# Kernel tuning notes

Hardware: AMD Instinct MI355X
Metric: run time of the kernel (lower is better)

Reference implementation:

```python
import jax, jax.numpy as jnp
import numpy as np

N = 10000      # nodes
E = 320000     # edges (before self loops)
IN = 256
HID = 64
H = 8
OUT = 64
NEG_SLOPE = 0.2


def setup_inputs() -> dict:
    key = jax.random.key(0)
    ks = jax.random.split(key, 12)
    def glorot(k, shape):
        fan = sum(shape) if len(shape) == 2 else int(np.prod(shape))
        return jax.random.normal(k, shape, jnp.float32) * np.sqrt(2.0 / fan)
    x = jax.random.normal(ks[0], (N, IN), jnp.float32)
    edge_index = jax.random.randint(ks[1], (2, E), 0, N, jnp.int32)
    # positive weights so log2 is finite
    edge_weight = jax.random.uniform(ks[2], (E,), jnp.float32, 0.1, 1.0)
    return {
        'x': x, 'edge_index': edge_index, 'edge_weight': edge_weight,
        'W1': glorot(ks[3], (IN, H * HID)),
        'as1': glorot(ks[4], (H, HID)), 'ad1': glorot(ks[5], (H, HID)),
        'b1': jnp.zeros((H * HID,), jnp.float32),
        'W2': glorot(ks[6], (H * HID, H * OUT)),
        'as2': glorot(ks[7], (H, OUT)), 'ad2': glorot(ks[8], (H, OUT)),
        'b2': jnp.zeros((H * OUT,), jnp.float32),
    }


def _gat_conv(x, src, dst, log2_ew, W, att_src, att_dst, bias, heads, ch):
    n = x.shape[0]
    h = (x @ W).reshape(n, heads, ch)                      # [N,H,C]
    al_src = jnp.einsum('nhc,hc->nh', h, att_src)          # [N,H]
    al_dst = jnp.einsum('nhc,hc->nh', h, att_dst)
    alpha = al_src[src] + al_dst[dst]                      # [E,H]
    alpha = jax.nn.leaky_relu(alpha, NEG_SLOPE)
    alpha = alpha + log2_ew[:, None]
    # segment softmax over destination nodes (self loops ensure nonempty segments)
    amax = jax.ops.segment_max(alpha, dst, num_segments=n)
    ex = jnp.exp(alpha - amax[dst])
    denom = jax.ops.segment_sum(ex, dst, num_segments=n)
    alpha = ex / denom[dst]                                # [E,H]
    msg = h[src] * alpha[:, :, None]                       # [E,H,C]
    out = jax.ops.segment_sum(msg, dst, num_segments=n)    # [N,H,C]
    return out.reshape(n, heads * ch) + bias


def reference(x, edge_index, edge_weight, W1, as1, ad1, b1, W2, as2, ad2, b2):
    n = x.shape[0]
    # add self loops with fill_value = 1.0 (log2(1) = 0)
    loops = jnp.arange(n, dtype=edge_index.dtype)
    src = jnp.concatenate([edge_index[0], loops])
    dst = jnp.concatenate([edge_index[1], loops])
    ew = jnp.concatenate([edge_weight, jnp.ones((n,), edge_weight.dtype)])
    log2_ew = jnp.log2(ew)
    h = _gat_conv(x, src, dst, log2_ew, W1, as1, ad1, b1, H, HID)
    h = jax.nn.relu(h)  # dropout skipped (eval mode)
    out = _gat_conv(h, src, dst, log2_ew, W2, as2, ad2, b2, H, OUT)
    return out
```

## Files before the change

### kernel.cpp

```cpp
#include <hip/hip_runtime.h>
#include <hip/hip_bf16.h>

#define NN 10000
#define EE 320000
#define ETOT (EE + NN)
#define CIN 256
#define HC 512
#define NHEAD 8
#define NEG 0.2f

#define SX (NN * CIN)
#define SATT (6 * 512)

using bf16x8 = __attribute__((ext_vector_type(8))) short;
using f32x4 = __attribute__((ext_vector_type(4))) float;
typedef unsigned short u16;
typedef unsigned int u32;

__device__ __forceinline__ u16 f2bf(float f) {
  __hip_bfloat16 b = __float2bfloat16(f);
  return *(u16*)&b;
}
__device__ __forceinline__ float bflo(u32 p) { return __uint_as_float(p << 16); }
__device__ __forceinline__ float bfhi(u32 p) { return __uint_as_float(p & 0xFFFF0000u); }

#define PB_X ((SX + 255) / 256)
#define PB_ATT ((SATT + 255) / 256)
#define PB_CNT ((ETOT + 255) / 256)
#define PB_WT 96
#define PB_TOT (PB_X + PB_ATT + PB_CNT + PB_WT)

__global__ __launch_bounds__(256) void prep_k(
    const void* __restrict__ x, const void* __restrict__ w1,
    const void* __restrict__ w2,
    const void* a0, const void* a1, const void* a2,
    const void* a3, const void* a4, const void* a5,
    const int* __restrict__ ei,
    u16* __restrict__ xb, u16* __restrict__ w1t, u16* __restrict__ w2t,
    float* __restrict__ attf, int* __restrict__ counts, int* __restrict__ flag) {
  const int b = blockIdx.x, t = threadIdx.x;
  __shared__ int sbad;
  if (t == 0) sbad = 0;
  __syncthreads();
  {
    const u16* xu = (const u16*)x;
    unsigned e0 = (xu[2 * t] >> 7) & 0xFFu;
    unsigned e1 = (xu[2 * t + 1] >> 7) & 0xFFu;
    if (e0 >= 0xC8u || e1 >= 0xC8u) sbad = 1;
  }
  __syncthreads();
  const bool bf = (sbad == 0);
  if (b == 0 && t == 0) *flag = bf ? 1 : 0;

  if (b < PB_X) {
    if (!bf) {
      int i = b * 256 + t;
      if (i < SX) xb[i] = f2bf(((const float*)x)[i]);
    }
  } else if (b < PB_X + PB_ATT) {
    int j = (b - PB_X) * 256 + t;
    if (j < SATT) {
      const void* ps[6] = {a0, a1, a2, a3, a4, a5};
      const void* p = ps[j >> 9];
      int k = j & 511;
      attf[j] = bf ? __bfloat162float(((const __hip_bfloat16*)p)[k])
                   : ((const float*)p)[k];
    }
  } else if (b < PB_X + PB_ATT + PB_CNT) {
    int e = (b - PB_X - PB_ATT) * 256 + t;
    if (e < ETOT) {
      int d = (e < EE) ? ei[EE + e] : (e - EE);
      atomicAdd(&counts[d], 1);
    }
  } else {
    __shared__ u16 tile[64][72];
    int wb = b - (PB_X + PB_ATT + PB_CNT);
    const void* src;
    u16* dst;
    int K, tk, tn;
    if (wb < 32) { src = w1; dst = w1t; K = CIN; tk = (wb >> 3) * 64; tn = (wb & 7) * 64; }
    else { wb -= 32; src = w2; dst = w2t; K = HC; tk = (wb >> 3) * 64; tn = (wb & 7) * 64; }
    const int r = t >> 2, cb = (t & 3) * 16;
    if (bf) {
      const u16* s = (const u16*)src + (size_t)(tk + r) * HC + tn + cb;
      *(int4*)&tile[r][cb] = ((const int4*)s)[0];
      *(int4*)&tile[r][cb + 8] = ((const int4*)s)[1];
    } else {
      const float* s = (const float*)src + (size_t)(tk + r) * HC + tn + cb;
#pragma unroll
      for (int j = 0; j < 16; j++) tile[r][cb + j] = f2bf(s[j]);
    }
    __syncthreads();
    union { u16 o[16]; int4 v[2]; } u;
#pragma unroll
    for (int j = 0; j < 16; j++) u.o[j] = tile[cb + j][r];
    int4* dp = (int4*)(dst + (size_t)(tn + r) * K + tk + cb);
    dp[0] = u.v[0];
    dp[1] = u.v[1];
  }
}

__global__ __launch_bounds__(1024) void scan_k(const int* __restrict__ counts,
                                               int* __restrict__ rowptr,
                                               int* __restrict__ wcur) {
  __shared__ int buf[1024];
  const int t = threadIdx.x;
  int loc[10];
  int s = 0;
#pragma unroll
  for (int j = 0; j < 10; j++) {
    int i = t * 10 + j;
    s += (i < NN) ? counts[i] : 0;
    loc[j] = s;
  }
  buf[t] = s;
  __syncthreads();
  for (int off = 1; off < 1024; off <<= 1) {
    int v = (t >= off) ? buf[t - off] : 0;
    __syncthreads();
    buf[t] += v;
    __syncthreads();
  }
  int base = (t > 0) ? buf[t - 1] : 0;
  int prev = 0;
#pragma unroll
  for (int j = 0; j < 10; j++) {
    int i = t * 10 + j;
    if (i < NN) {
      rowptr[i + 1] = base + loc[j];
      wcur[i] = base + prev;
    }
    prev = loc[j];
  }
  if (t == 0) rowptr[0] = 0;
}

__global__ void fill_k(const int* __restrict__ ei, const void* __restrict__ ew,
                       const int* __restrict__ flag, int* __restrict__ wcur,
                       int* __restrict__ esrc, float* __restrict__ elw) {
  int e = blockIdx.x * blockDim.x + threadIdx.x;
  if (e >= ETOT) return;
  int s, d;
  float lw;
  if (e < EE) {
    s = ei[e];
    d = ei[EE + e];
    float w = (*flag) ? __bfloat162float(((const __hip_bfloat16*)ew)[e])
                      : ((const float*)ew)[e];
    lw = log2f(w);
  } else {
    s = d = e - EE;
    lw = 0.f;
  }
  int pos = atomicAdd(&wcur[d], 1);
  esrc[pos] = s;
  elw[pos] = lw;
}

#define BM 64
#define BN 128
#define BK 64
#define LSTR 72

__global__ __launch_bounds__(256) void gemm_mfma(const u16* __restrict__ A,
                                                 const void* __restrict__ Axalt,
                                                 const int* __restrict__ flagp,
                                                 const u16* __restrict__ Wt,
                                                 const float* __restrict__ as_w,
                                                 const float* __restrict__ ad_w,
                                                 u16* __restrict__ hb,
                                                 float* __restrict__ alsrc,
                                                 float* __restrict__ aldst,
                                                 int M, int K) {
  __shared__ u16 As[BM * LSTR];
  __shared__ u16 Bs[BN * LSTR];
  __shared__ float sps[2][2][BM], spd[2][2][BM];
  const u16* Asel = (flagp && *flagp) ? (const u16*)Axalt : A;
  const int bx = blockIdx.x;
  const int bm = blockIdx.y * BM, bn = bx * BN;
  const int t = threadIdx.x, wv = t >> 6, lane = t & 63;
  const int l15 = lane & 15, quad = lane >> 4;
  f32x4 acc[4][2] = {};
  for (int k0 = 0; k0 < K; k0 += BK) {
    {
      int row = t >> 2, kq = (t & 3) * 16;
      int gr = bm + row;
      int4 v0 = make_int4(0, 0, 0, 0), v1 = v0;
      if (gr < M) {
        const int4* gp = (const int4*)(Asel + (size_t)gr * K + k0 + kq);
        v0 = gp[0];
        v1 = gp[1];
      }
      int4* lp = (int4*)(As + row * LSTR + kq);
      lp[0] = v0;
      lp[1] = v1;
    }
    {
      int row = t >> 1, kq = (t & 1) * 32;
      const int4* gp = (const int4*)(Wt + (size_t)(bn + row) * K + k0 + kq);
      int4* lp = (int4*)(Bs + row * LSTR + kq);
      lp[0] = gp[0];
      lp[1] = gp[1];
      lp[2] = gp[2];
      lp[3] = gp[3];
    }
    __syncthreads();
#pragma unroll
    for (int kk = 0; kk < 2; kk++) {
      bf16x8 bfr[2];
#pragma unroll
      for (int ct = 0; ct < 2; ct++)
        bfr[ct] = *(const bf16x8*)(Bs + (wv * 32 + ct * 16 + l15) * LSTR + kk * 32 + quad * 8);
#pragma unroll
      for (int rt = 0; rt < 4; rt++) {
        bf16x8 af = *(const bf16x8*)(As + (rt * 16 + l15) * LSTR + kk * 32 + quad * 8);
#pragma unroll
        for (int ct = 0; ct < 2; ct++)
          acc[rt][ct] = __builtin_amdgcn_mfma_f32_16x16x32_bf16(af, bfr[ct],
                                                                acc[rt][ct], 0, 0, 0);
      }
    }
    __syncthreads();
  }
  const int head = bx * 2 + (wv >> 1);
  float asw[2], adw[2];
#pragma unroll
  for (int ct = 0; ct < 2; ct++) {
    int c = head * 64 + (wv & 1) * 32 + ct * 16 + l15;
    asw[ct] = as_w[c];
    adw[ct] = ad_w[c];
  }
#pragma unroll
  for (int rt = 0; rt < 4; rt++) {
#pragma unroll
    for (int r = 0; r < 4; r++) {
      int rib = rt * 16 + quad * 4 + r;
      int row = bm + rib;
      float ps = 0.f, pd = 0.f;
#pragma unroll
      for (int ct = 0; ct < 2; ct++) {
        float v = acc[rt][ct][r];
        ps += v * asw[ct];
        pd += v * adw[ct];
        if (row < M)
          hb[(size_t)row * HC + bn + wv * 32 + ct * 16 + l15] = f2bf(v);
      }
#pragma unroll
      for (int d = 1; d < 16; d <<= 1) {
        ps += __shfl_xor(ps, d);
        pd += __shfl_xor(pd, d);
      }
      if (l15 == 0) {
        sps[wv >> 1][wv & 1][rib] = ps;
        spd[wv >> 1][wv & 1][rib] = pd;
      }
    }
  }
  __syncthreads();
  if (t < 2 * BM) {
    int rib = t & 63, hs = t >> 6;
    int row = bm + rib;
    if (row < M) {
      alsrc[row * NHEAD + bx * 2 + hs] = sps[hs][0][rib] + sps[hs][1][rib];
      aldst[row * NHEAD + bx * 2 + hs] = spd[hs][0][rib] + spd[hs][1][rib];
    }
  }
}

#define ACC8(P, W)                                                             \
  {                                                                            \
    const u32 q0 = (u32)(P).x, q1 = (u32)(P).y, q2 = (u32)(P).z, q3 = (u32)(P).w; \
    acc[0] += (W)*bflo(q0);                                                    \
    acc[1] += (W)*bfhi(q0);                                                    \
    acc[2] += (W)*bflo(q1);                                                    \
    acc[3] += (W)*bfhi(q1);                                                    \
    acc[4] += (W)*bflo(q2);                                                    \
    acc[5] += (W)*bfhi(q2);                                                    \
    acc[6] += (W)*bflo(q3);                                                    \
    acc[7] += (W)*bfhi(q3);                                                    \
  }

template <bool RELU, bool FINAL>
__global__ __launch_bounds__(256) void agg_k(const u16* __restrict__ hb,
                                             const float* __restrict__ alsrc,
                                             const float* __restrict__ aldst,
                                             const int* __restrict__ rowptr,
                                             const int* __restrict__ esrc,
                                             const float* __restrict__ elw,
                                             const float* __restrict__ bias,
                                             u32* __restrict__ outB,
                                             float* __restrict__ outF,
                                             const int* __restrict__ flag) {
  const int t = threadIdx.x;
  const int wv = t >> 6, lane = t & 63;
  const int n = blockIdx.x * 4 + wv;
  const int h = lane & 7, eo = lane >> 3;
  const int hh = lane >> 3;
  const int chbase = lane * 8;
  __shared__ float swA[4][NHEAD][132];
  __shared__ int ssA[4][128];
  float (*const swv)[132] = swA[wv];
  int* const ssv = ssA[wv];
  const int beg = rowptr[n];
  const int deg = rowptr[n + 1] - beg;
  const float aln = aldst[(size_t)n * NHEAD + h];
  float acc[8] = {};
  float inv;

  if (deg <= 128) {
    float m = -1e30f;
    for (int j = eo; j < deg; j += 8) {
      int e = beg + j;
      int s = esrc[e];
      float a = alsrc[(size_t)s * NHEAD + h] + aln;
      a = (a > 0.f) ? a : NEG * a;
      a += elw[e];
      swv[h][j] = a;
      m = fmaxf(m, a);
      if (h == 0) ssv[j] = s;
    }
    m = fmaxf(m, __shfl_xor(m, 8));
    m = fmaxf(m, __shfl_xor(m, 16));
    m = fmaxf(m, __shfl_xor(m, 32));
    float sum = 0.f;
    for (int j = eo; j < deg; j += 8) {
      float w = expf(swv[h][j] - m);
      swv[h][j] = w;
      sum += w;
    }
    sum += __shfl_xor(sum, 8);
    sum += __shfl_xor(sum, 16);
    sum += __shfl_xor(sum, 32);
    inv = 1.f / __shfl(sum, hh);
    int i = 0;
    for (; i + 3 < deg; i += 4) {
      const int s0 = ssv[i], s1 = ssv[i + 1], s2 = ssv[i + 2], s3 = ssv[i + 3];
      const float w0 = swv[hh][i], w1 = swv[hh][i + 1];
      const float w2 = swv[hh][i + 2], w3 = swv[hh][i + 3];
      const int4 p0 = *(const int4*)(hb + (size_t)s0 * HC + chbase);
      const int4 p1 = *(const int4*)(hb + (size_t)s1 * HC + chbase);
      const int4 p2 = *(const int4*)(hb + (size_t)s2 * HC + chbase);
      const int4 p3 = *(const int4*)(hb + (size_t)s3 * HC + chbase);
      ACC8(p0, w0)
      ACC8(p1, w1)
      ACC8(p2, w2)
      ACC8(p3, w3)
    }
    for (; i < deg; i++) {
      const int s = ssv[i];
      const float w = swv[hh][i];
      const int4 p = *(const int4*)(hb + (size_t)s * HC + chbase);
      ACC8(p, w)
    }
  } else {
    float m = -1e30f;
    for (int j = eo; j < deg; j += 8) {
      int e = beg + j;
      float a = alsrc[(size_t)esrc[e] * NHEAD + h] + aln;
      a = (a > 0.f) ? a : NEG * a;
      m = fmaxf(m, a + elw[e]);
    }
    m = fmaxf(m, __shfl_xor(m, 8));
    m = fmaxf(m, __shfl_xor(m, 16));
    m = fmaxf(m, __shfl_xor(m, 32));
    float sum = 0.f;
    for (int j = eo; j < deg; j += 8) {
      int e = beg + j;
      float a = alsrc[(size_t)esrc[e] * NHEAD + h] + aln;
      a = (a > 0.f) ? a : NEG * a;
      sum += expf(a + elw[e] - m);
    }
    sum += __shfl_xor(sum, 8);
    sum += __shfl_xor(sum, 16);
    sum += __shfl_xor(sum, 32);
    inv = 1.f / __shfl(sum, hh);
    const float mh = __shfl(m, hh);
    const float alnh = __shfl(aln, hh);
    for (int i = 0; i < deg; i++) {
      int e = beg + i;
      int s = esrc[e];
      float a = alsrc[(size_t)s * NHEAD + hh] + alnh;
      a = (a > 0.f) ? a : NEG * a;
      float w = expf(a + elw[e] - mh);
      const int4 p = *(const int4*)(hb + (size_t)s * HC + chbase);
      ACC8(p, w)
    }
  }
  const float4 b0 = *(const float4*)(bias + chbase);
  const float4 b1 = *(const float4*)(bias + chbase + 4);
  float v[8];
  v[0] = acc[0] * inv + b0.x; v[1] = acc[1] * inv + b0.y;
  v[2] = acc[2] * inv + b0.z; v[3] = acc[3] * inv + b0.w;
  v[4] = acc[4] * inv + b1.x; v[5] = acc[5] * inv + b1.y;
  v[6] = acc[6] * inv + b1.z; v[7] = acc[7] * inv + b1.w;
  if (RELU) {
#pragma unroll
    for (int k = 0; k < 8; k++) v[k] = fmaxf(v[k], 0.f);
  }
  if (FINAL && !(*flag)) {
    float4* op = (float4*)(outF + (size_t)n * HC + chbase);
    op[0] = make_float4(v[0], v[1], v[2], v[3]);
    op[1] = make_float4(v[4], v[5], v[6], v[7]);
  } else {
    int4 pk;
    pk.x = (int)((u32)f2bf(v[0]) | ((u32)f2bf(v[1]) << 16));
    pk.y = (int)((u32)f2bf(v[2]) | ((u32)f2bf(v[3]) << 16));
    pk.z = (int)((u32)f2bf(v[4]) | ((u32)f2bf(v[5]) << 16));
    pk.w = (int)((u32)f2bf(v[6]) | ((u32)f2bf(v[7]) << 16));
    *(int4*)(outB + (size_t)n * (HC / 2) + lane * 4) = pk;
  }
}

static constexpr size_t algn(size_t x) { return (x + 255) & ~(size_t)255; }
static constexpr size_t oFlag = 0;
static constexpr size_t oXB = algn(oFlag + 256);
static constexpr size_t oW1T = algn(oXB + (size_t)SX * 2);
static constexpr size_t oW2T = algn(oW1T + (size_t)CIN * HC * 2);
static constexpr size_t oAtt = algn(oW2T + (size_t)HC * HC * 2);
static constexpr size_t oHB = algn(oAtt + (size_t)SATT * 4);
static constexpr size_t oO1B = algn(oHB + (size_t)NN * HC * 2);
static constexpr size_t oAS = algn(oO1B + (size_t)NN * HC * 2);
static constexpr size_t oAD = algn(oAS + (size_t)NN * NHEAD * 4);
static constexpr size_t oRP = algn(oAD + (size_t)NN * NHEAD * 4);
static constexpr size_t oCnt = algn(oRP + (size_t)(NN + 1) * 4);
static constexpr size_t oWcur = algn(oCnt + (size_t)NN * 4);
static constexpr size_t oESrc = algn(oWcur + (size_t)NN * 4);
static constexpr size_t oELW = algn(oESrc + (size_t)ETOT * 4);

extern "C" void kernel_launch(void* const* d_in, const int* in_sizes, int n_in,
                              void* d_out, int out_size, void* d_ws, size_t ws_size,
                              hipStream_t stream) {
  (void)in_sizes; (void)n_in; (void)out_size; (void)ws_size;
  const int* ei = (const int*)d_in[1];

  char* ws = (char*)d_ws;
  int* flag = (int*)(ws + oFlag);
  u16* xb = (u16*)(ws + oXB);
  u16* w1t = (u16*)(ws + oW1T);
  u16* w2t = (u16*)(ws + oW2T);
  float* attf = (float*)(ws + oAtt);
  float* as1f = attf, *ad1f = attf + 512, *b1f = attf + 1024;
  float* as2f = attf + 1536, *ad2f = attf + 2048, *b2f = attf + 2560;
  u16* hb = (u16*)(ws + oHB);
  u16* o1b = (u16*)(ws + oO1B);
  float* alsrc = (float*)(ws + oAS);
  float* aldst = (float*)(ws + oAD);
  int* rowptr = (int*)(ws + oRP);
  int* counts = (int*)(ws + oCnt);
  int* wcur = (int*)(ws + oWcur);
  int* esrc = (int*)(ws + oESrc);
  float* elw = (float*)(ws + oELW);

  hipMemsetAsync(counts, 0, (size_t)NN * 4, stream);
  prep_k<<<PB_TOT, 256, 0, stream>>>(d_in[0], d_in[3], d_in[7],
                                     d_in[4], d_in[5], d_in[6],
                                     d_in[8], d_in[9], d_in[10], ei,
                                     xb, w1t, w2t, attf, counts, flag);
  scan_k<<<1, 1024, 0, stream>>>(counts, rowptr, wcur);
  fill_k<<<(ETOT + 255) / 256, 256, 0, stream>>>(ei, d_in[2], flag, wcur, esrc, elw);

  gemm_mfma<<<dim3(HC / BN, (NN + BM - 1) / BM), 256, 0, stream>>>(
      xb, d_in[0], flag, w1t, as1f, ad1f, hb, alsrc, aldst, NN, CIN);
  agg_k<true, false><<<NN / 4, 256, 0, stream>>>(hb, alsrc, aldst, rowptr, esrc, elw,
                                                 b1f, (u32*)o1b, nullptr, flag);

  gemm_mfma<<<dim3(HC / BN, (NN + BM - 1) / BM), 256, 0, stream>>>(
      o1b, nullptr, nullptr, w2t, as2f, ad2f, hb, alsrc, aldst, NN, HC);
  agg_k<false, true><<<NN / 4, 256, 0, stream>>>(hb, alsrc, aldst, rowptr, esrc, elw,
                                                 b2f, (u32*)d_out, (float*)d_out, flag);
}
```

Measured before the change: 259.4 us.

## Bucket CSR edges by source range to improve gather locality

Builds the CSR with eight source-node buckets per destination, so edges in each row come out roughly sorted by source id. The goal is better cache locality when the aggregation kernels gather h rows and alsrc entries. In exchange the counts, rowptr and cursor arrays grow eightfold, and the single-block scan now walks 80000 entries serially at 79 per thread.

Measured after the change: 434.7 us. +67.6%, slower.

```diff
diff --git a/kernel.cpp b/kernel.cpp
--- a/kernel.cpp
+++ b/kernel.cpp
@@ -8,6 +8,8 @@
 #define HC 512
 #define NHEAD 8
 #define NEG 0.2f
+#define NBKT 8
+#define BKTW 1250
 
 #define SX (NN * CIN)
 #define SATT (6 * 512)
@@ -69,8 +71,11 @@
   } else if (b < PB_X + PB_ATT + PB_CNT) {
     int e = (b - PB_X - PB_ATT) * 256 + t;
     if (e < ETOT) {
-      int d = (e < EE) ? ei[EE + e] : (e - EE);
-      atomicAdd(&counts[d], 1);
+      int d, s;
+      if (e < EE) { s = ei[e]; d = ei[EE + e]; }
+      else { s = d = e - EE; }
+      int q = s / BKTW;
+      atomicAdd(&counts[d * NBKT + q], 1);
     }
   } else {
     __shared__ u16 tile[64][72];
@@ -100,18 +105,18 @@
   }
 }
 
+#define SCNT (NBKT * NN)
+#define SPER 79
+
 __global__ __launch_bounds__(1024) void scan_k(const int* __restrict__ counts,
-                                               int* __restrict__ rowptr,
+                                               int* __restrict__ rowptr4,
                                                int* __restrict__ wcur) {
   __shared__ int buf[1024];
   const int t = threadIdx.x;
-  int loc[10];
   int s = 0;
-#pragma unroll
-  for (int j = 0; j < 10; j++) {
-    int i = t * 10 + j;
-    s += (i < NN) ? counts[i] : 0;
-    loc[j] = s;
+  for (int j = 0; j < SPER; j++) {
+    int i = t * SPER + j;
+    if (i < SCNT) s += counts[i];
   }
   buf[t] = s;
   __syncthreads();
@@ -121,18 +126,16 @@
     buf[t] += v;
     __syncthreads();
   }
-  int base = (t > 0) ? buf[t - 1] : 0;
-  int prev = 0;
-#pragma unroll
-  for (int j = 0; j < 10; j++) {
-    int i = t * 10 + j;
-    if (i < NN) {
-      rowptr[i + 1] = base + loc[j];
-      wcur[i] = base + prev;
-    }
-    prev = loc[j];
-  }
-  if (t == 0) rowptr[0] = 0;
+  int run = (t > 0) ? buf[t - 1] : 0;
+  for (int j = 0; j < SPER; j++) {
+    int i = t * SPER + j;
+    if (i < SCNT) {
+      rowptr4[i] = run;
+      wcur[i] = run;
+      run += counts[i];
+    }
+  }
+  if (t == 1023) rowptr4[SCNT] = buf[1023];
 }
 
 __global__ void fill_k(const int* __restrict__ ei, const void* __restrict__ ew,
@@ -152,7 +155,8 @@
     s = d = e - EE;
     lw = 0.f;
   }
-  int pos = atomicAdd(&wcur[d], 1);
+  int q = s / BKTW;
+  int pos = atomicAdd(&wcur[d * NBKT + q], 1);
   esrc[pos] = s;
   elw[pos] = lw;
 }
@@ -284,7 +288,7 @@
 __global__ __launch_bounds__(256) void agg_k(const u16* __restrict__ hb,
                                              const float* __restrict__ alsrc,
                                              const float* __restrict__ aldst,
-                                             const int* __restrict__ rowptr,
+                                             const int* __restrict__ rowptr4,
                                              const int* __restrict__ esrc,
                                              const float* __restrict__ elw,
                                              const float* __restrict__ bias,
@@ -301,8 +305,8 @@
   __shared__ int ssA[4][128];
   float (*const swv)[132] = swA[wv];
   int* const ssv = ssA[wv];
-  const int beg = rowptr[n];
-  const int deg = rowptr[n + 1] - beg;
+  const int beg = rowptr4[n * NBKT];
+  const int deg = rowptr4[n * NBKT + NBKT] - beg;
   const float aln = aldst[(size_t)n * NHEAD + h];
   float acc[8] = {};
   float inv;
@@ -421,10 +425,10 @@
 static constexpr size_t oO1B = algn(oHB + (size_t)NN * HC * 2);
 static constexpr size_t oAS = algn(oO1B + (size_t)NN * HC * 2);
 static constexpr size_t oAD = algn(oAS + (size_t)NN * NHEAD * 4);
-static constexpr size_t oRP = algn(oAD + (size_t)NN * NHEAD * 4);
-static constexpr size_t oCnt = algn(oRP + (size_t)(NN + 1) * 4);
-static constexpr size_t oWcur = algn(oCnt + (size_t)NN * 4);
-static constexpr size_t oESrc = algn(oWcur + (size_t)NN * 4);
+static constexpr size_t oCnt = algn(oAD + (size_t)NN * NHEAD * 4);
+static constexpr size_t oRP4 = algn(oCnt + (size_t)SCNT * 4);
+static constexpr size_t oWcur = algn(oRP4 + (size_t)(SCNT + 1) * 4);
+static constexpr size_t oESrc = algn(oWcur + (size_t)SCNT * 4);
 static constexpr size_t oELW = algn(oESrc + (size_t)ETOT * 4);
 
 extern "C" void kernel_launch(void* const* d_in, const int* in_sizes, int n_in,
@@ -445,27 +449,27 @@
   u16* o1b = (u16*)(ws + oO1B);
   float* alsrc = (float*)(ws + oAS);
   float* aldst = (float*)(ws + oAD);
-  int* rowptr = (int*)(ws + oRP);
   int* counts = (int*)(ws + oCnt);
+  int* rowptr4 = (int*)(ws + oRP4);
   int* wcur = (int*)(ws + oWcur);
   int* esrc = (int*)(ws + oESrc);
   float* elw = (float*)(ws + oELW);
 
-  hipMemsetAsync(counts, 0, (size_t)NN * 4, stream);
+  hipMemsetAsync(counts, 0, (size_t)SCNT * 4, stream);
   prep_k<<<PB_TOT, 256, 0, stream>>>(d_in[0], d_in[3], d_in[7],
                                      d_in[4], d_in[5], d_in[6],
                                      d_in[8], d_in[9], d_in[10], ei,
                                      xb, w1t, w2t, attf, counts, flag);
-  scan_k<<<1, 1024, 0, stream>>>(counts, rowptr, wcur);
+  scan_k<<<1, 1024, 0, stream>>>(counts, rowptr4, wcur);
   fill_k<<<(ETOT + 255) / 256, 256, 0, stream>>>(ei, d_in[2], flag, wcur, esrc, elw);
 
   gemm_mfma<<<dim3(HC / BN, (NN + BM - 1) / BM), 256, 0, stream>>>(
       xb, d_in[0], flag, w1t, as1f, ad1f, hb, alsrc, aldst, NN, CIN);
-  agg_k<true, false><<<NN / 4, 256, 0, stream>>>(hb, alsrc, aldst, rowptr, esrc, elw,
+  agg_k<true, false><<<NN / 4, 256, 0, stream>>>(hb, alsrc, aldst, rowptr4, esrc, elw,
                                                  b1f, (u32*)o1b, nullptr, flag);
 
   gemm_mfma<<<dim3(HC / BN, (NN + BM - 1) / BM), 256, 0, stream>>>(
       o1b, nullptr, nullptr, w2t, as2f, ad2f, hb, alsrc, aldst, NN, HC);
-  agg_k<false, true><<<NN / 4, 256, 0, stream>>>(hb, alsrc, aldst, rowptr, esrc, elw,
+  agg_k<false, true><<<NN / 4, 256, 0, stream>>>(hb, alsrc, aldst, rowptr4, esrc, elw,
                                                  b2f, (u32*)d_out, (float*)d_out, flag);
 }
```
